# Kernel tuning notes

Hardware: AMD Instinct MI355X
Metric: run time of the kernel (lower is better)

The kernel has to match this reference:

```python
import jax, jax.numpy as jnp
import numpy as np

IN_C, OUT_C, EDGE_C = 128, 64, 1
N_NODES, N_EDGES = 50000, 800000


def setup_inputs() -> dict:
    key = jax.random.key(0)
    ks = jax.random.split(key, 12)
    d = OUT_C
    # xavier-uniform-ish scales
    def xav(k, shape):
        lim = float(np.sqrt(6.0 / (shape[0] + shape[1])))
        return jax.random.uniform(k, shape, jnp.float32, -lim, lim)
    return {
        "feat_src": jax.random.normal(ks[0], (N_NODES, IN_C), jnp.float32),
        "feat_dst": jax.random.normal(ks[1], (N_NODES, IN_C), jnp.float32),
        "edge_weight": jax.random.uniform(ks[2], (N_EDGES, EDGE_C), jnp.float32),
        "src_idx": jax.random.randint(ks[3], (N_EDGES,), 0, N_NODES),
        "dst_idx": jnp.sort(jax.random.randint(ks[4], (N_EDGES,), 0, N_NODES)),
        "weight_n": xav(ks[5], (IN_C, d)),
        "weight_e": xav(ks[6], (EDGE_C, d)),
        "query": xav(ks[7], (d, d)),
        "key_w": xav(ks[8], (d, d)),
        "att_w": xav(ks[9], (3 * d, 1)),
        "att_b": jnp.zeros((1,), jnp.float32),
        "out_w": xav(ks[10], (2 * d, d)),
        "out_b": jnp.zeros((d,), jnp.float32),
    }


def reference(feat_src, feat_dst, edge_weight, src_idx, dst_idx,
              weight_n, weight_e, query, key_w, att_w, att_b, out_w, out_b):
    d = query.shape[0]
    n_dst = feat_dst.shape[0]
    h_src = feat_src @ weight_n                      # [N_src, d]
    h_dst = feat_dst @ weight_n                      # [N_dst, d]
    edge_emb = edge_weight @ weight_e                # [E, d]
    q_e = (h_dst @ query)[dst_idx]                   # [E, d] gather
    k_e = (h_src @ key_w)[src_idx]                   # [E, d] gather
    # linear_att(concat([q, k, e])) without materializing the concat
    logits = (q_e @ att_w[:d] + k_e @ att_w[d:2 * d]
              + edge_emb @ att_w[2 * d:] + att_b)    # [E, 1]
    logits = jax.nn.leaky_relu(logits, 0.2)
    # segment softmax over destination nodes
    m = jax.ops.segment_max(logits, dst_idx, num_segments=n_dst)   # [N_dst, 1]
    ex = jnp.exp(logits - m[dst_idx])
    s = jax.ops.segment_sum(ex, dst_idx, num_segments=n_dst)       # [N_dst, 1]
    alpha = ex / (s[dst_idx] + 1e-16)                # [E, 1]
    msg = alpha * h_src[src_idx]                     # [E, d]
    agg = jax.ops.segment_sum(msg, dst_idx, num_segments=n_dst)    # [N_dst, d]
    # linear_out(concat([h_dst, agg]))
    out = h_dst @ out_w[:d] + agg @ out_w[d:] + out_b
    return out
```

## Files before the change

kernel.cpp:

```cpp
#include <hip/hip_runtime.h>
#include <hip/hip_bf16.h>

typedef short short8 __attribute__((ext_vector_type(8)));
typedef float float4v __attribute__((ext_vector_type(4)));
typedef unsigned short ushort4v __attribute__((ext_vector_type(4)));

static __device__ __forceinline__ short f2b(float f) {
    union { __hip_bfloat16 b; short s; } v;
    v.b = __float2bfloat16(f);
    return v.s;
}
static __device__ __forceinline__ float b2f(unsigned short u) {
    union { float f; unsigned v; } x;
    x.v = ((unsigned)u) << 16;
    return x.f;
}

__global__ void prep_a_kernel(const float* __restrict__ query, const float* __restrict__ key_w,
                              const float* __restrict__ weight_e, const float* __restrict__ att_w,
                              float* __restrict__ qa, float* __restrict__ ka,
                              float* __restrict__ escale) {
    int i = threadIdx.x;
    float sq = 0.f, sk = 0.f;
    for (int j = 0; j < 64; ++j) {
        sq += query[i * 64 + j] * att_w[j];
        sk += key_w[i * 64 + j] * att_w[64 + j];
    }
    qa[i] = sq;
    ka[i] = sk;
    float e = weight_e[i] * att_w[128 + i];
    for (int off = 32; off; off >>= 1) e += __shfl_xor(e, off);
    if (i == 0) escale[0] = e;
}

__global__ void prep_w_kernel(const float* __restrict__ Wn, const float* __restrict__ out_w,
                              const float* __restrict__ ka, const float* __restrict__ qa,
                              float* __restrict__ W1p, float* __restrict__ W2p,
                              float* __restrict__ Wk, float* __restrict__ Wq) {
    int idx = blockIdx.x * 256 + threadIdx.x;
    if (idx < 16384) {
        int mat = idx >> 13;
        int rem = idx & 8191;
        int i = rem >> 6, j = rem & 63;
        float s = 0.f;
        for (int k = 0; k < 64; ++k)
            s += Wn[i * 64 + k] * out_w[(mat * 64 + k) * 64 + j];
        (mat ? W2p : W1p)[i * 64 + j] = s;
    } else if (idx < 16384 + 256) {
        int r = idx - 16384;
        int i = r & 127;
        const float* v = (r < 128) ? ka : qa;
        float s = 0.f;
        for (int k = 0; k < 64; ++k) s += Wn[i * 64 + k] * v[k];
        (r < 128 ? Wk : Wq)[i] = s;
    }
}

__global__ void rowptr_kernel(const int* __restrict__ dst_idx, int* __restrict__ row_ptr,
                              int n_nodes, int n_edges) {
    int t = blockIdx.x * blockDim.x + threadIdx.x;
    if (t > n_nodes) return;
    int lo = 0, hi = n_edges;
    while (lo < hi) {
        int mid = (lo + hi) >> 1;
        if (dst_idx[mid] < t) lo = mid + 1; else hi = mid;
    }
    row_ptr[t] = lo;
}

template <bool BF16OUT>
__global__ void __launch_bounds__(256) gemm_kernel(
    const float* __restrict__ A, const float* __restrict__ B,
    unsigned short* __restrict__ Cb, float* __restrict__ Cf,
    const float* __restrict__ bias, const float* __restrict__ w,
    float* __restrict__ sc, int M) {
    __shared__ __align__(16) short BT[64 * 136];
    int t = threadIdx.x;
#pragma unroll
    for (int i = 0; i < 32; ++i) {
        int idx = i * 256 + t;
        int k = idx >> 6, n = idx & 63;
        BT[n * 136 + k] = f2b(B[idx]);
    }
    __syncthreads();

    int wave = t >> 6, lane = t & 63;
    int m15 = lane & 15, quad = lane >> 4;
#pragma unroll
    for (int tile = 0; tile < 2; ++tile) {
        int rb = blockIdx.x * 128 + wave * 32 + tile * 16;
        if (rb >= M) continue;
        const float* Arow = A + (size_t)(rb + m15) * 128 + quad * 8;

        float4v acc[4] = {};
        float sk = 0.f;
#pragma unroll
        for (int kk = 0; kk < 4; ++kk) {
            float4v a0 = *(const float4v*)(Arow + kk * 32);
            float4v a1 = *(const float4v*)(Arow + kk * 32 + 4);
            float4v w0 = *(const float4v*)(w + kk * 32 + quad * 8);
            float4v w1 = *(const float4v*)(w + kk * 32 + quad * 8 + 4);
#pragma unroll
            for (int j = 0; j < 4; ++j) sk += a0[j] * w0[j] + a1[j] * w1[j];
            short8 a;
#pragma unroll
            for (int j = 0; j < 4; ++j) { a[j] = f2b(a0[j]); a[4 + j] = f2b(a1[j]); }
#pragma unroll
            for (int nt = 0; nt < 4; ++nt) {
                short8 b = *(const short8*)(&BT[(nt * 16 + m15) * 136 + kk * 32 + quad * 8]);
                acc[nt] = __builtin_amdgcn_mfma_f32_16x16x32_bf16(a, b, acc[nt], 0, 0, 0);
            }
        }

#pragma unroll
        for (int nt = 0; nt < 4; ++nt) {
            int col = nt * 16 + m15;
            float bv = BF16OUT ? 0.f : bias[col];
#pragma unroll
            for (int r = 0; r < 4; ++r) {
                int row = rb + quad * 4 + r;
                if (BF16OUT) Cb[(size_t)row * 64 + col] = (unsigned short)f2b(acc[nt][r]);
                else         Cf[(size_t)row * 64 + col] = acc[nt][r] + bv;
            }
        }
        sk += __shfl_xor(sk, 16);
        sk += __shfl_xor(sk, 32);
        if (quad == 0) sc[rb + m15] = sk;
    }
}

__global__ void __launch_bounds__(256) agg_kernel(
    const int* __restrict__ src_idx, const float* __restrict__ edge_w,
    const unsigned short* __restrict__ hw2, const float* __restrict__ kscore,
    const float* __restrict__ qscore, const float* __restrict__ escale_p,
    const float* __restrict__ att_b, const int* __restrict__ row_ptr,
    float* __restrict__ out, int n_nodes) {
    int wave = (int)((blockIdx.x * blockDim.x + threadIdx.x) >> 6);
    int lane = threadIdx.x & 63;
    if (wave >= n_nodes) return;
    int n = wave;
    int start = row_ptr[n];
    int end = row_ptr[n + 1];
    int deg = end - start;
    int eslot = lane >> 4;
    int cg = lane & 15;

    float ac0 = 0.f, ac1 = 0.f, ac2 = 0.f, ac3 = 0.f;
    if (deg > 0) {
        float escale = escale_p[0];
        float bias = att_b[0];
        float qs = qscore[n];

        float mx = -1e30f, sm = 0.f;
        int s0 = 0; float lg0 = -1e30f;
        for (int eo = lane; eo < deg; eo += 64) {
            int s = src_idx[start + eo];
            float lg = qs + kscore[s] + edge_w[start + eo] * escale + bias;
            lg = (lg > 0.f) ? lg : 0.2f * lg;
            if (eo == lane) { s0 = s; lg0 = lg; }
            float nm = fmaxf(mx, lg);
            sm = sm * __expf(mx - nm) + __expf(lg - nm);
            mx = nm;
        }
        for (int off = 32; off; off >>= 1) {
            float m2 = __shfl_xor(mx, off);
            float s2 = __shfl_xor(sm, off);
            float nm = fmaxf(mx, m2);
            sm = sm * __expf(mx - nm) + s2 * __expf(m2 - nm);
            mx = nm;
        }
        float inv = 1.f / (sm + 1e-16f);

        if (deg <= 64) {
            float alpha0 = __expf(lg0 - mx) * inv;
            for (int base = 0; base < deg; base += 4) {
                int eo = base + eslot;
                bool valid = eo < deg;
                int idx = valid ? eo : 0;
                float alpha = __shfl(alpha0, idx);
                int s = __shfl(s0, idx);
                if (!valid) alpha = 0.f;
                ushort4v h = *(const ushort4v*)(hw2 + (size_t)s * 64 + cg * 4);
                ac0 += alpha * b2f(h[0]);
                ac1 += alpha * b2f(h[1]);
                ac2 += alpha * b2f(h[2]);
                ac3 += alpha * b2f(h[3]);
            }
        } else {
            for (int base = 0; base < deg; base += 4) {
                int eo = base + eslot;
                bool valid = eo < deg;
                int e = start + (valid ? eo : 0);
                int s = src_idx[e];
                float lg = qs + kscore[s] + edge_w[e] * escale + bias;
                lg = (lg > 0.f) ? lg : 0.2f * lg;
                float alpha = valid ? __expf(lg - mx) * inv : 0.f;
                ushort4v h = *(const ushort4v*)(hw2 + (size_t)s * 64 + cg * 4);
                ac0 += alpha * b2f(h[0]);
                ac1 += alpha * b2f(h[1]);
                ac2 += alpha * b2f(h[2]);
                ac3 += alpha * b2f(h[3]);
            }
        }
        ac0 += __shfl_xor(ac0, 16); ac0 += __shfl_xor(ac0, 32);
        ac1 += __shfl_xor(ac1, 16); ac1 += __shfl_xor(ac1, 32);
        ac2 += __shfl_xor(ac2, 16); ac2 += __shfl_xor(ac2, 32);
        ac3 += __shfl_xor(ac3, 16); ac3 += __shfl_xor(ac3, 32);
    }
    if (lane < 16) {
        float4v b = *(const float4v*)(out + (size_t)n * 64 + lane * 4);
        b[0] += ac0; b[1] += ac1; b[2] += ac2; b[3] += ac3;
        *(float4v*)(out + (size_t)n * 64 + lane * 4) = b;
    }
}

extern "C" void kernel_launch(void* const* d_in, const int* in_sizes, int n_in,
                              void* d_out, int out_size, void* d_ws, size_t ws_size,
                              hipStream_t stream) {
    const float* feat_src = (const float*)d_in[0];
    const float* feat_dst = (const float*)d_in[1];
    const float* edge_w   = (const float*)d_in[2];
    const int*   src_idx  = (const int*)d_in[3];
    const int*   dst_idx  = (const int*)d_in[4];
    const float* weight_n = (const float*)d_in[5];
    const float* weight_e = (const float*)d_in[6];
    const float* query    = (const float*)d_in[7];
    const float* key_w    = (const float*)d_in[8];
    const float* att_w    = (const float*)d_in[9];
    const float* att_b    = (const float*)d_in[10];
    const float* out_w    = (const float*)d_in[11];
    const float* out_b    = (const float*)d_in[12];
    float* out = (float*)d_out;

    int n_nodes = in_sizes[0] / 128;
    int n_edges = in_sizes[3];

    char* p = (char*)d_ws;
    unsigned short* hw2 = (unsigned short*)p;  p += (size_t)n_nodes * 64 * 2;
    float* kscore = (float*)p;  p += (size_t)n_nodes * 4;
    float* qscore = (float*)p;  p += (size_t)n_nodes * 4;
    float* W1p    = (float*)p;  p += 128 * 64 * 4;
    float* W2p    = (float*)p;  p += 128 * 64 * 4;
    float* Wk     = (float*)p;  p += 128 * 4;
    float* Wq     = (float*)p;  p += 128 * 4;
    float* qa     = (float*)p;  p += 64 * 4;
    float* ka     = (float*)p;  p += 64 * 4;
    float* escale = (float*)p;  p += 64;
    int*  row_ptr = (int*)p;

    hipLaunchKernelGGL(prep_a_kernel, dim3(1), dim3(64), 0, stream,
                       query, key_w, weight_e, att_w, qa, ka, escale);

    hipLaunchKernelGGL(prep_w_kernel, dim3(65), dim3(256), 0, stream,
                       weight_n, out_w, ka, qa, W1p, W2p, Wk, Wq);

    hipLaunchKernelGGL(rowptr_kernel, dim3((n_nodes + 256) / 256), dim3(256), 0, stream,
                       dst_idx, row_ptr, n_nodes, n_edges);

    int g_blocks = (n_nodes + 127) / 128;
    hipLaunchKernelGGL((gemm_kernel<true>), dim3(g_blocks), dim3(256), 0, stream,
                       feat_src, W2p, hw2, (float*)nullptr, (const float*)nullptr,
                       Wk, kscore, n_nodes);
    hipLaunchKernelGGL((gemm_kernel<false>), dim3(g_blocks), dim3(256), 0, stream,
                       feat_dst, W1p, (unsigned short*)nullptr, out, out_b,
                       Wq, qscore, n_nodes);

    hipLaunchKernelGGL(agg_kernel, dim3((n_nodes + 3) / 4), dim3(256), 0, stream,
                       src_idx, edge_w, hw2, kscore, qscore,
                       escale, att_b, row_ptr, out, n_nodes);
}
```

Before: 169.4 us.

## Merge prep kernels, fuse src/dst GEMMs into one launch, simplify softmax

Three setup kernels (attention vectors, weight products, row pointers) become one kernel with block roles, and the two node GEMMs are combined into a single launch over 2*N rows, with each block picking source or destination weights. In the aggregation kernel, low-degree nodes now compute the softmax with one load per lane and plain max and sum reductions instead of an online loop. The goal is fewer launches and less serial setup, at the cost of extra shared memory in the GEMM, which may lower occupancy.

```diff
diff --git a/kernel.cpp b/kernel.cpp
--- a/kernel.cpp
+++ b/kernel.cpp
@@ -16,29 +16,17 @@
     return x.f;
 }
 
-__global__ void prep_a_kernel(const float* __restrict__ query, const float* __restrict__ key_w,
-                              const float* __restrict__ weight_e, const float* __restrict__ att_w,
-                              float* __restrict__ qa, float* __restrict__ ka,
-                              float* __restrict__ escale) {
-    int i = threadIdx.x;
-    float sq = 0.f, sk = 0.f;
-    for (int j = 0; j < 64; ++j) {
-        sq += query[i * 64 + j] * att_w[j];
-        sk += key_w[i * 64 + j] * att_w[64 + j];
-    }
-    qa[i] = sq;
-    ka[i] = sk;
-    float e = weight_e[i] * att_w[128 + i];
-    for (int off = 32; off; off >>= 1) e += __shfl_xor(e, off);
-    if (i == 0) escale[0] = e;
-}
-
-__global__ void prep_w_kernel(const float* __restrict__ Wn, const float* __restrict__ out_w,
-                              const float* __restrict__ ka, const float* __restrict__ qa,
-                              float* __restrict__ W1p, float* __restrict__ W2p,
-                              float* __restrict__ Wk, float* __restrict__ Wq) {
-    int idx = blockIdx.x * 256 + threadIdx.x;
-    if (idx < 16384) {
+__global__ void __launch_bounds__(256) setup_kernel(
+    const float* __restrict__ query, const float* __restrict__ key_w,
+    const float* __restrict__ weight_e, const float* __restrict__ att_w,
+    const float* __restrict__ Wn, const float* __restrict__ out_w,
+    const int* __restrict__ dst_idx,
+    float* __restrict__ W1p, float* __restrict__ W2p,
+    float* __restrict__ Wk, float* __restrict__ Wq, float* __restrict__ escale,
+    int* __restrict__ row_ptr, int n_nodes, int n_edges) {
+    int b = blockIdx.x, t = threadIdx.x;
+    if (b < 64) {
+        int idx = b * 256 + t;
         int mat = idx >> 13;
         int rem = idx & 8191;
         int i = rem >> 6, j = rem & 63;
@@ -46,41 +34,79 @@
         for (int k = 0; k < 64; ++k)
             s += Wn[i * 64 + k] * out_w[(mat * 64 + k) * 64 + j];
         (mat ? W2p : W1p)[i * 64 + j] = s;
-    } else if (idx < 16384 + 256) {
-        int r = idx - 16384;
-        int i = r & 127;
-        const float* v = (r < 128) ? ka : qa;
-        float s = 0.f;
-        for (int k = 0; k < 64; ++k) s += Wn[i * 64 + k] * v[k];
-        (r < 128 ? Wk : Wq)[i] = s;
-    }
-}
-
-__global__ void rowptr_kernel(const int* __restrict__ dst_idx, int* __restrict__ row_ptr,
-                              int n_nodes, int n_edges) {
-    int t = blockIdx.x * blockDim.x + threadIdx.x;
-    if (t > n_nodes) return;
-    int lo = 0, hi = n_edges;
-    while (lo < hi) {
-        int mid = (lo + hi) >> 1;
-        if (dst_idx[mid] < t) lo = mid + 1; else hi = mid;
-    }
-    row_ptr[t] = lo;
-}
-
-template <bool BF16OUT>
+    } else if (b == 64) {
+        __shared__ float kq[128];
+        __shared__ float ep[64];
+        if (t < 64) {
+            float s = 0.f;
+            for (int j = 0; j < 64; ++j) s += key_w[t * 64 + j] * att_w[64 + j];
+            kq[t] = s;
+        } else if (t < 128) {
+            int i = t - 64;
+            float s = 0.f;
+            for (int j = 0; j < 64; ++j) s += query[i * 64 + j] * att_w[j];
+            kq[64 + i] = s;
+        } else if (t < 192) {
+            int j = t - 128;
+            ep[j] = weight_e[j] * att_w[128 + j];
+        }
+        __syncthreads();
+        if (t < 128) {
+            float s = 0.f;
+            for (int k = 0; k < 64; ++k) s += Wn[t * 64 + k] * kq[k];
+            Wk[t] = s;
+        } else {
+            int i = t - 128;
+            float s = 0.f;
+            for (int k = 0; k < 64; ++k) s += Wn[i * 64 + k] * kq[64 + k];
+            Wq[i] = s;
+        }
+        if (t == 0) {
+            float s = 0.f;
+            for (int j = 0; j < 64; ++j) s += ep[j];
+            escale[0] = s;
+        }
+    } else {
+        int idx = (b - 65) * 256 + t;
+        if (idx > n_nodes) return;
+        int lo = 0, hi = n_edges;
+        while (lo < hi) {
+            int mid = (lo + hi) >> 1;
+            if (dst_idx[mid] < idx) lo = mid + 1; else hi = mid;
+        }
+        row_ptr[idx] = lo;
+    }
+}
+
 __global__ void __launch_bounds__(256) gemm_kernel(
-    const float* __restrict__ A, const float* __restrict__ B,
-    unsigned short* __restrict__ Cb, float* __restrict__ Cf,
-    const float* __restrict__ bias, const float* __restrict__ w,
-    float* __restrict__ sc, int M) {
-    __shared__ __align__(16) short BT[64 * 136];
+    const float* __restrict__ feat_src, const float* __restrict__ feat_dst,
+    const float* __restrict__ W2p, const float* __restrict__ W1p,
+    const float* __restrict__ Wk, const float* __restrict__ Wq,
+    unsigned short* __restrict__ hw2, float* __restrict__ out,
+    const float* __restrict__ out_b, float* __restrict__ kscore,
+    float* __restrict__ qscore, int n_nodes) {
+    __shared__ __align__(16) short BTs[64 * 136];
+    __shared__ __align__(16) short BTd[64 * 136];
     int t = threadIdx.x;
-#pragma unroll
-    for (int i = 0; i < 32; ++i) {
-        int idx = i * 256 + t;
-        int k = idx >> 6, n = idx & 63;
-        BT[n * 136 + k] = f2b(B[idx]);
+    int row0 = blockIdx.x * 128;
+    int total = 2 * n_nodes;
+    bool needS = row0 < n_nodes;
+    bool needD = row0 + 127 >= n_nodes;
+    if (needS) {
+#pragma unroll
+        for (int i = 0; i < 32; ++i) {
+            int idx = i * 256 + t;
+            int k = idx >> 6, n = idx & 63;
+            BTs[n * 136 + k] = f2b(W2p[idx]);
+        }
+    }
+    if (needD) {
+#pragma unroll
+        for (int i = 0; i < 32; ++i) {
+            int idx = i * 256 + t;
+            int k = idx >> 6, n = idx & 63;
+            BTd[n * 136 + k] = f2b(W1p[idx]);
+        }
     }
     __syncthreads();
 
@@ -88,9 +114,14 @@
     int m15 = lane & 15, quad = lane >> 4;
 #pragma unroll
     for (int tile = 0; tile < 2; ++tile) {
-        int rb = blockIdx.x * 128 + wave * 32 + tile * 16;
-        if (rb >= M) continue;
-        const float* Arow = A + (size_t)(rb + m15) * 128 + quad * 8;
+        int rb = row0 + wave * 32 + tile * 16;
+        if (rb >= total) continue;
+        bool isSrc = rb < n_nodes;
+        const float* Arow = (isSrc ? feat_src + (size_t)rb * 128
+                                   : feat_dst + (size_t)(rb - n_nodes) * 128)
+                            + (size_t)m15 * 128 + quad * 8;
+        const short* BT = isSrc ? BTs : BTd;
+        const float* w = isSrc ? Wk : Wq;
 
         float4v acc[4] = {};
         float sk = 0.f;
@@ -107,25 +138,28 @@
             for (int j = 0; j < 4; ++j) { a[j] = f2b(a0[j]); a[4 + j] = f2b(a1[j]); }
 #pragma unroll
             for (int nt = 0; nt < 4; ++nt) {
-                short8 b = *(const short8*)(&BT[(nt * 16 + m15) * 136 + kk * 32 + quad * 8]);
-                acc[nt] = __builtin_amdgcn_mfma_f32_16x16x32_bf16(a, b, acc[nt], 0, 0, 0);
+                short8 bb = *(const short8*)(&BT[(nt * 16 + m15) * 136 + kk * 32 + quad * 8]);
+                acc[nt] = __builtin_amdgcn_mfma_f32_16x16x32_bf16(a, bb, acc[nt], 0, 0, 0);
             }
         }
 
 #pragma unroll
         for (int nt = 0; nt < 4; ++nt) {
             int col = nt * 16 + m15;
-            float bv = BF16OUT ? 0.f : bias[col];
+            float bv = isSrc ? 0.f : out_b[col];
 #pragma unroll
             for (int r = 0; r < 4; ++r) {
                 int row = rb + quad * 4 + r;
-                if (BF16OUT) Cb[(size_t)row * 64 + col] = (unsigned short)f2b(acc[nt][r]);
-                else         Cf[(size_t)row * 64 + col] = acc[nt][r] + bv;
+                if (isSrc) hw2[(size_t)row * 64 + col] = (unsigned short)f2b(acc[nt][r]);
+                else       out[(size_t)(row - n_nodes) * 64 + col] = acc[nt][r] + bv;
             }
         }
         sk += __shfl_xor(sk, 16);
         sk += __shfl_xor(sk, 32);
-        if (quad == 0) sc[rb + m15] = sk;
+        if (quad == 0) {
+            if (isSrc) kscore[rb + m15] = sk;
+            else       qscore[rb + m15 - n_nodes] = sk;
+        }
     }
 }
 
@@ -140,8 +174,7 @@
     if (wave >= n_nodes) return;
     int n = wave;
     int start = row_ptr[n];
-    int end = row_ptr[n + 1];
-    int deg = end - start;
+    int deg = row_ptr[n + 1] - start;
     int eslot = lane >> 4;
     int cg = lane & 15;
 
@@ -151,35 +184,28 @@
         float bias = att_b[0];
         float qs = qscore[n];
 
-        float mx = -1e30f, sm = 0.f;
-        int s0 = 0; float lg0 = -1e30f;
-        for (int eo = lane; eo < deg; eo += 64) {
-            int s = src_idx[start + eo];
-            float lg = qs + kscore[s] + edge_w[start + eo] * escale + bias;
-            lg = (lg > 0.f) ? lg : 0.2f * lg;
-            if (eo == lane) { s0 = s; lg0 = lg; }
-            float nm = fmaxf(mx, lg);
-            sm = sm * __expf(mx - nm) + __expf(lg - nm);
-            mx = nm;
-        }
-        for (int off = 32; off; off >>= 1) {
-            float m2 = __shfl_xor(mx, off);
-            float s2 = __shfl_xor(sm, off);
-            float nm = fmaxf(mx, m2);
-            sm = sm * __expf(mx - nm) + s2 * __expf(m2 - nm);
-            mx = nm;
-        }
-        float inv = 1.f / (sm + 1e-16f);
-
         if (deg <= 64) {
-            float alpha0 = __expf(lg0 - mx) * inv;
+            int s0 = 0; float lg0 = -1e30f;
+            if (lane < deg) {
+                s0 = src_idx[start + lane];
+                float lg = qs + kscore[s0] + edge_w[start + lane] * escale + bias;
+                lg0 = (lg > 0.f) ? lg : 0.2f * lg;
+            }
+            float mx = lg0;
+#pragma unroll
+            for (int off = 32; off; off >>= 1) mx = fmaxf(mx, __shfl_xor(mx, off));
+            float a0 = __expf(lg0 - mx);
+            float sm = a0;
+#pragma unroll
+            for (int off = 32; off; off >>= 1) sm += __shfl_xor(sm, off);
+            float alpha0 = a0 * (1.f / (sm + 1e-16f));
+
             for (int base = 0; base < deg; base += 4) {
                 int eo = base + eslot;
-                bool valid = eo < deg;
-                int idx = valid ? eo : 0;
+                int idx = (eo < deg) ? eo : 0;
                 float alpha = __shfl(alpha0, idx);
                 int s = __shfl(s0, idx);
-                if (!valid) alpha = 0.f;
+                if (eo >= deg) alpha = 0.f;
                 ushort4v h = *(const ushort4v*)(hw2 + (size_t)s * 64 + cg * 4);
                 ac0 += alpha * b2f(h[0]);
                 ac1 += alpha * b2f(h[1]);
@@ -187,6 +213,23 @@
                 ac3 += alpha * b2f(h[3]);
             }
         } else {
+            float mx = -1e30f, sm = 0.f;
+            for (int eo = lane; eo < deg; eo += 64) {
+                int s = src_idx[start + eo];
+                float lg = qs + kscore[s] + edge_w[start + eo] * escale + bias;
+                lg = (lg > 0.f) ? lg : 0.2f * lg;
+                float nm = fmaxf(mx, lg);
+                sm = sm * __expf(mx - nm) + __expf(lg - nm);
+                mx = nm;
+            }
+            for (int off = 32; off; off >>= 1) {
+                float m2 = __shfl_xor(mx, off);
+                float s2 = __shfl_xor(sm, off);
+                float nm = fmaxf(mx, m2);
+                sm = sm * __expf(mx - nm) + s2 * __expf(m2 - nm);
+                mx = nm;
+            }
+            float inv = 1.f / (sm + 1e-16f);
             for (int base = 0; base < deg; base += 4) {
                 int eo = base + eslot;
                 bool valid = eo < deg;
@@ -243,27 +286,18 @@
     float* W2p    = (float*)p;  p += 128 * 64 * 4;
     float* Wk     = (float*)p;  p += 128 * 4;
     float* Wq     = (float*)p;  p += 128 * 4;
-    float* qa     = (float*)p;  p += 64 * 4;
-    float* ka     = (float*)p;  p += 64 * 4;
     float* escale = (float*)p;  p += 64;
     int*  row_ptr = (int*)p;
 
-    hipLaunchKernelGGL(prep_a_kernel, dim3(1), dim3(64), 0, stream,
-                       query, key_w, weight_e, att_w, qa, ka, escale);
-
-    hipLaunchKernelGGL(prep_w_kernel, dim3(65), dim3(256), 0, stream,
-                       weight_n, out_w, ka, qa, W1p, W2p, Wk, Wq);
-
-    hipLaunchKernelGGL(rowptr_kernel, dim3((n_nodes + 256) / 256), dim3(256), 0, stream,
-                       dst_idx, row_ptr, n_nodes, n_edges);
-
-    int g_blocks = (n_nodes + 127) / 128;
-    hipLaunchKernelGGL((gemm_kernel<true>), dim3(g_blocks), dim3(256), 0, stream,
-                       feat_src, W2p, hw2, (float*)nullptr, (const float*)nullptr,
-                       Wk, kscore, n_nodes);
-    hipLaunchKernelGGL((gemm_kernel<false>), dim3(g_blocks), dim3(256), 0, stream,
-                       feat_dst, W1p, (unsigned short*)nullptr, out, out_b,
-                       Wq, qscore, n_nodes);
+    int rp_blocks = (n_nodes + 1 + 255) / 256;
+    hipLaunchKernelGGL(setup_kernel, dim3(65 + rp_blocks), dim3(256), 0, stream,
+                       query, key_w, weight_e, att_w, weight_n, out_w, dst_idx,
+                       W1p, W2p, Wk, Wq, escale, row_ptr, n_nodes, n_edges);
+
+    int g_blocks = (2 * n_nodes + 127) / 128;
+    hipLaunchKernelGGL(gemm_kernel, dim3(g_blocks), dim3(256), 0, stream,
+                       feat_src, feat_dst, W2p, W1p, Wk, Wq,
+                       hw2, out, out_b, kscore, qscore, n_nodes);
 
     hipLaunchKernelGGL(agg_kernel, dim3((n_nodes + 3) / 4), dim3(256), 0, stream,
                        src_idx, edge_w, hw2, kscore, qscore,
```

After: 164.7 us. 2.8% less time.
